# Optimization experiments

Hardware: AMD Instinct MI355X
Metric: run time of the kernel (lower is better)

## Reference

```python
import jax, jax.numpy as jnp
import numpy as np

HW, B, C, NH, NC, HF, WF = 2500, 2, 256, 8, 6, 64, 176
DFF = 4 * C
EPS = 1e-5

def _layernorm(x, g, b):
    m = x.mean(-1, keepdims=True)
    v = ((x - m) ** 2).mean(-1, keepdims=True)
    return (x - m) / jnp.sqrt(v + EPS) * g + b

def _mha(q, kv, in_w, in_b, ow, ob):
    # q: [L,B,C], kv: [S,B,C] (batch_first=False, torch nn.MultiheadAttention)
    L, Bq, Cq = q.shape
    S = kv.shape[0]
    Dh = Cq // NH
    qp = (q @ in_w[:Cq].T + in_b[:Cq]).reshape(L, Bq, NH, Dh)
    kp = (kv @ in_w[Cq:2 * Cq].T + in_b[Cq:2 * Cq]).reshape(S, Bq, NH, Dh)
    vp = (kv @ in_w[2 * Cq:].T + in_b[2 * Cq:]).reshape(S, Bq, NH, Dh)
    att = jnp.einsum('lbhd,sbhd->bhls', qp, kp) * (1.0 / np.sqrt(Dh))
    att = jax.nn.softmax(att, axis=-1)
    out = jnp.einsum('bhls,sbhd->lbhd', att, vp).reshape(L, Bq, Cq)
    return out @ ow.T + ob

def _grid_sample_zeros(feat, grid):
    # feat: [B,N,C,H,W], grid: [B,N,Q,2] in [-1,1]; bilinear, align_corners=False, zero padding
    Bb, N, Cc, Hf, Wf = feat.shape
    Q = grid.shape[2]
    x = (grid[..., 0] + 1.0) * (Wf / 2.0) - 0.5
    y = (grid[..., 1] + 1.0) * (Hf / 2.0) - 0.5
    x0 = jnp.floor(x); y0 = jnp.floor(y)
    wx = x - x0; wy = y - y0
    x0i = x0.astype(jnp.int32); y0i = y0.astype(jnp.int32)
    ff = feat.reshape(Bb, N, Cc, Hf * Wf)
    def corner(xi, yi, w):
        valid = (xi >= 0) & (xi < Wf) & (yi >= 0) & (yi < Hf)
        idx = jnp.clip(yi, 0, Hf - 1) * Wf + jnp.clip(xi, 0, Wf - 1)  # [B,N,Q]
        g = jnp.take_along_axis(ff, jnp.broadcast_to(idx[:, :, None, :], (Bb, N, Cc, Q)), axis=-1)
        return g * (w * valid)[:, :, None, :]
    return (corner(x0i, y0i, (1.0 - wx) * (1.0 - wy)) + corner(x0i + 1, y0i, wx * (1.0 - wy))
            + corner(x0i, y0i + 1, (1.0 - wx) * wy) + corner(x0i + 1, y0i + 1, wx * wy))

def _forward(bev_queries, prev_bev, image_feat, reference_points, camera_intrinsics, camera_extrinsics,
             in_proj_w, in_proj_b, out_proj_w, out_proj_b, tsa_norm_g, tsa_norm_b,
             sca_w, sca_b, sca_norm_g, sca_norm_b, ffn_w1, ffn_b1, ffn_w2, ffn_b2, ffn_norm_g, ffn_norm_b):
    # TSA (dropout is identity in eval)
    tsa_out = _mha(bev_queries, prev_bev, in_proj_w, in_proj_b, out_proj_w, out_proj_b)
    x = _layernorm(bev_queries + tsa_out, tsa_norm_g, tsa_norm_b)
    # SCA: ego->camera->image projection
    R = camera_extrinsics[:, :, :3, :3]            # [B,N,3,3]
    t = camera_extrinsics[:, :, :3, 3]             # [B,N,3]
    R_e2c = jnp.swapaxes(R, -1, -2)
    t_e2c = -jnp.einsum('bnij,bnj->bni', R_e2c, t)
    pts_cam = jnp.einsum('bnij,qj->bnqi', R_e2c, reference_points) + t_e2c[:, :, None, :]  # [B,N,Q,3]
    pts_img = jnp.einsum('bnij,bnqj->bnqi', camera_intrinsics, pts_cam)
    uv = pts_img[..., :2] / jnp.maximum(pts_img[..., 2:3], 1e-5)
    grid = jnp.stack([2.0 * uv[..., 0] / WF - 1.0, 2.0 * uv[..., 1] / HF - 1.0], axis=-1)  # [B,N,Q,2]
    Bq = bev_queries.shape[1]
    feat_r = image_feat.reshape(Bq, NC, C, HF, WF)
    sampled = _grid_sample_zeros(feat_r, grid).mean(axis=1)   # [B,C,Q]
    sampled = jnp.transpose(sampled, (2, 0, 1))               # [Q,B,C]
    sca_out = sampled @ sca_w.T + sca_b
    x = _layernorm(x + sca_out, sca_norm_g, sca_norm_b)
    # FFN (torch nn.GELU default = exact erf)
    h = jax.nn.gelu(x @ ffn_w1 + ffn_b1, approximate=False)
    ffn_out = h @ ffn_w2 + ffn_b2
    return _layernorm(x + ffn_out, ffn_norm_g, ffn_norm_b)

def setup_inputs():
    key = jax.random.key(0)
    ks = jax.random.split(key, 16)
    f = jnp.float32
    s = 0.02
    return {
        'bev_queries': jax.random.normal(ks[0], (HW, B, C), f),
        'prev_bev': jax.random.normal(ks[1], (HW, B, C), f),
        'image_feat': jax.random.normal(ks[2], (B * NC, C, HF, WF), f),
        'reference_points': jax.random.normal(ks[3], (HW, 3), f) * 20.0,
        'camera_intrinsics': jax.random.normal(ks[4], (B, NC, 3, 3), f),
        'camera_extrinsics': jax.random.normal(ks[5], (B, NC, 4, 4), f),
        'spatial_shapes': jnp.array([[HF, WF]], jnp.int32),
        'in_proj_w': jax.random.normal(ks[6], (3 * C, C), f) * s,
        'in_proj_b': jnp.zeros((3 * C,), f),
        'out_proj_w': jax.random.normal(ks[7], (C, C), f) * s,
        'out_proj_b': jnp.zeros((C,), f),
        'tsa_norm_g': jnp.ones((C,), f), 'tsa_norm_b': jnp.zeros((C,), f),
        'sca_w': jax.random.normal(ks[8], (C, C), f) * s,
        'sca_b': jnp.zeros((C,), f),
        'sca_norm_g': jnp.ones((C,), f), 'sca_norm_b': jnp.zeros((C,), f),
        'ffn_w1': jax.random.normal(ks[9], (C, DFF), f) * s,
        'ffn_b1': jnp.zeros((DFF,), f),
        'ffn_w2': jax.random.normal(ks[10], (DFF, C), f) * s,
        'ffn_b2': jnp.zeros((C,), f),
        'ffn_norm_g': jnp.ones((C,), f), 'ffn_norm_b': jnp.zeros((C,), f),
    }

def reference(bev_queries, prev_bev, image_feat, reference_points, camera_intrinsics, camera_extrinsics,
              in_proj_w, in_proj_b, out_proj_w, out_proj_b, tsa_norm_g, tsa_norm_b,
              sca_w, sca_b, sca_norm_g, sca_norm_b, ffn_w1, ffn_b1, ffn_w2, ffn_b2, ffn_norm_g, ffn_norm_b,
              spatial_shapes):
    return _forward(bev_queries, prev_bev, image_feat, reference_points, camera_intrinsics, camera_extrinsics,
                    in_proj_w, in_proj_b, out_proj_w, out_proj_b, tsa_norm_g, tsa_norm_b,
                    sca_w, sca_b, sca_norm_g, sca_norm_b, ffn_w1, ffn_b1, ffn_w2, ffn_b2, ffn_norm_g, ffn_norm_b)
```

## Files before the change

### kernel.cpp

```cpp
#include <hip/hip_runtime.h>

typedef unsigned short u16;
typedef __attribute__((ext_vector_type(8))) __bf16 bf8_t;
typedef __attribute__((ext_vector_type(4))) float f4_t;

__device__ __forceinline__ float bf2f(u16 v) {
  return __uint_as_float(((unsigned int)v) << 16);
}
__device__ __forceinline__ u16 f2bf(float f) {
  unsigned int u = __float_as_uint(f);
  unsigned int r = u + 0x7FFFu + ((u >> 16) & 1u);
  return (u16)(r >> 16);
}
__device__ __forceinline__ float bflo(unsigned int w) { return __uint_as_float(w << 16); }
__device__ __forceinline__ float bfhi(unsigned int w) { return __uint_as_float(w & 0xFFFF0000u); }

__device__ __forceinline__ void load8(const void* base, size_t off, int isf32, float v[8]) {
  if (isf32) {
    const float* p = (const float*)base + off;
    float4 a = *(const float4*)p, b = *(const float4*)(p + 4);
    v[0]=a.x; v[1]=a.y; v[2]=a.z; v[3]=a.w; v[4]=b.x; v[5]=b.y; v[6]=b.z; v[7]=b.w;
  } else {
    uint4 r = *(const uint4*)((const u16*)base + off);
    v[0]=bflo(r.x); v[1]=bfhi(r.x); v[2]=bflo(r.y); v[3]=bfhi(r.y);
    v[4]=bflo(r.z); v[5]=bfhi(r.z); v[6]=bflo(r.w); v[7]=bfhi(r.w);
  }
}
__device__ __forceinline__ float ldf1(const void* p, size_t i, int isf32) {
  return isf32 ? ((const float*)p)[i] : bf2f(((const u16*)p)[i]);
}

#define LQ   2500
#define BB   2
#define CC   256
#define DH   32
#define NCC  6
#define HFF  64
#define WFF  176
#define DFF  1024
#define MROWS 5000

#define WB_UV   256
#define WB_WQKV 240256
#define WB_WOP  633472
#define WB_WSC  764544
#define WB_WF1  895616
#define WB_WF2  1419904
#define WB_S1   1944192
#define WB_S2   (WB_S1 + 2621440)
#define WB_S3   (WB_S2 + 2621440)
#define WB_S4   (WB_S3 + 2621440)
#define WB_H    WB_S2
#define WB_Y3   (WB_S2 + 10485760)

__global__ void detect_k(const u16* __restrict__ rp, int* __restrict__ flag) {
  int bad = 0;
  for (int i = threadIdx.x; i < 7500; i += 64) {
    float v = bf2f(rp[i]);
    if (!(fabsf(v) < 1e6f)) bad = 1;
  }
  int anybad = __any(bad);
  if (threadIdx.x == 0) flag[0] = anybad ? 1 : 0;
}

struct WDesc {
  const void* src[5];
  u16* dst[5];
  int n[5];
  int mode[5];
  int Kd[5], Nd[5];
};
__global__ __launch_bounds__(256) void cvtw_k(WDesc d, const int* __restrict__ flag) {
  const int df = flag[0];
  const int i = blockIdx.y;
  const int n = d.n[i];
  for (int j = blockIdx.x * 256 + threadIdx.x; j < n; j += gridDim.x * 256) {
    float v;
    if (d.mode[i]) {
      const int K = d.Kd[i], N = d.Nd[i];
      const int nn = j / K, kk = j - nn * K;
      v = ldf1(d.src[i], (size_t)kk * N + nn, df);
    } else {
      v = ldf1(d.src[i], j, df);
    }
    d.dst[i][j] = f2bf(v);
  }
}

template<int XRAW, int ACT, int RES>
__global__ __launch_bounds__(256) void gemm_mf(
    const void* __restrict__ Xv, const u16* __restrict__ W,
    const void* __restrict__ bias, size_t boff,
    const void* __restrict__ resv,
    u16* __restrict__ Y, int M, int N, int K, const int* __restrict__ flag)
{
  const int df = flag[0];
  const int xf = XRAW ? df : 0;
  __shared__ __align__(16) u16 sA[64 * 32];
  __shared__ __align__(16) u16 sB[64 * 32];
  const int t = threadIdx.x;
  const int m0 = blockIdx.y * 64, n0 = blockIdx.x * 64;
  const int lane = t & 63, w = t >> 6;
  const int wr = w >> 1, wc = w & 1;
  const int ln15 = lane & 15, l4 = lane >> 4;

  f4_t acc[2][2];
#pragma unroll
  for (int a = 0; a < 2; ++a)
#pragma unroll
    for (int bq = 0; bq < 2; ++bq) acc[a][bq] = (f4_t){0.f, 0.f, 0.f, 0.f};

  const int srow = t >> 2, scol = (t & 3) * 8;
  for (int k0 = 0; k0 < K; k0 += 32) {
    {
      const int gm = m0 + srow;
      float v[8] = {0.f,0.f,0.f,0.f,0.f,0.f,0.f,0.f};
      if (gm < M) load8(Xv, (size_t)gm * K + k0 + scol, xf, v);
      uint4 o;
      o.x = (unsigned int)f2bf(v[0]) | ((unsigned int)f2bf(v[1]) << 16);
      o.y = (unsigned int)f2bf(v[2]) | ((unsigned int)f2bf(v[3]) << 16);
      o.z = (unsigned int)f2bf(v[4]) | ((unsigned int)f2bf(v[5]) << 16);
      o.w = (unsigned int)f2bf(v[6]) | ((unsigned int)f2bf(v[7]) << 16);
      *(uint4*)&sA[srow * 32 + scol] = o;
    }
    *(uint4*)&sB[srow * 32 + scol] =
        *(const uint4*)&W[(size_t)(n0 + srow) * K + k0 + scol];
    __syncthreads();
    bf8_t af[2], bf_[2];
    af[0]  = *(const bf8_t*)&sA[(wr * 32 + 0  + ln15) * 32 + l4 * 8];
    af[1]  = *(const bf8_t*)&sA[(wr * 32 + 16 + ln15) * 32 + l4 * 8];
    bf_[0] = *(const bf8_t*)&sB[(wc * 32 + 0  + ln15) * 32 + l4 * 8];
    bf_[1] = *(const bf8_t*)&sB[(wc * 32 + 16 + ln15) * 32 + l4 * 8];
#pragma unroll
    for (int mt = 0; mt < 2; ++mt)
#pragma unroll
      for (int nt = 0; nt < 2; ++nt)
        acc[mt][nt] = __builtin_amdgcn_mfma_f32_16x16x32_bf16(af[mt], bf_[nt], acc[mt][nt], 0, 0, 0);
    __syncthreads();
  }
#pragma unroll
  for (int nt = 0; nt < 2; ++nt) {
    const int gn = n0 + wc * 32 + nt * 16 + ln15;
    const float bv = ldf1(bias, boff + gn, df);
#pragma unroll
    for (int mt = 0; mt < 2; ++mt)
#pragma unroll
      for (int r = 0; r < 4; ++r) {
        const int gm = m0 + wr * 32 + mt * 16 + l4 * 4 + r;
        if (gm < M) {
          float x = acc[mt][nt][r] + bv;
          if (ACT) x = 0.5f * x * (1.f + erff(x * 0.70710678118654752f));
          if (RES == 1)      x += bf2f(((const u16*)resv)[(size_t)gm * N + gn]);
          else if (RES == 2) x += ldf1(resv, (size_t)gm * N + gn, df);
          Y[(size_t)gm * N + gn] = f2bf(x);
        }
      }
  }
}

__global__ __launch_bounds__(256) void attn_mf(
    const u16* __restrict__ Qw, const u16* __restrict__ Kw,
    const u16* __restrict__ Vw, u16* __restrict__ Ow)
{
  __shared__ __align__(16) u16 sQ[64 * 32];
  __shared__ __align__(16) u16 sK[64 * 32];
  __shared__ __align__(16) u16 sVT[32 * 72];
  __shared__ __align__(16) u16 sP[64 * 72];
  const int t = threadIdx.x;
  const int q0 = blockIdx.x * 64;
  const int b = blockIdx.y >> 3, h = blockIdx.y & 7;
  const int lane = t & 63, w = t >> 6;
  const int ln15 = lane & 15, l4 = lane >> 4;
  const float SC = 0.17677669529663687f;

  {
    const int qi = t >> 2, dcol = (t & 3) * 8;
    const size_t src = ((size_t)(q0 + qi) * BB + b) * CC + h * DH + dcol;
    *(uint4*)&sQ[qi * 32 + dcol] = *(const uint4*)&Qw[src];
  }

  f4_t oacc[2];
  oacc[0] = (f4_t){0.f,0.f,0.f,0.f};
  oacc[1] = (f4_t){0.f,0.f,0.f,0.f};
  float m_r[4] = {-1e30f, -1e30f, -1e30f, -1e30f};
  float l_r[4] = {0.f, 0.f, 0.f, 0.f};
  __syncthreads();

  for (int kt = 0; kt < 40; ++kt) {
    const int kbase = kt * 64;
    {
      const int j = t >> 2, dcol = (t & 3) * 8;
      const size_t src = ((size_t)(kbase + j) * BB + b) * CC + h * DH + dcol;
      *(uint4*)&sK[j * 32 + dcol] = *(const uint4*)&Kw[src];
      uint4 vv = *(const uint4*)&Vw[src];
      u16 ve[8];
      ve[0] = (u16)(vv.x & 0xffff); ve[1] = (u16)(vv.x >> 16);
      ve[2] = (u16)(vv.y & 0xffff); ve[3] = (u16)(vv.y >> 16);
      ve[4] = (u16)(vv.z & 0xffff); ve[5] = (u16)(vv.z >> 16);
      ve[6] = (u16)(vv.w & 0xffff); ve[7] = (u16)(vv.w >> 16);
#pragma unroll
      for (int x = 0; x < 8; ++x) sVT[(dcol + x) * 72 + j] = ve[x];
    }
    __syncthreads();

    bf8_t aq = *(const bf8_t*)&sQ[(w * 16 + ln15) * 32 + l4 * 8];
    f4_t sv[4];
#pragma unroll
    for (int nt = 0; nt < 4; ++nt) {
      bf8_t bk = *(const bf8_t*)&sK[(nt * 16 + ln15) * 32 + l4 * 8];
      f4_t z = (f4_t){0.f,0.f,0.f,0.f};
      sv[nt] = __builtin_amdgcn_mfma_f32_16x16x32_bf16(aq, bk, z, 0, 0, 0);
    }

    float p[4][4];
#pragma unroll
    for (int nt = 0; nt < 4; ++nt) {
      const bool ok = (kbase + nt * 16 + ln15) < LQ;
#pragma unroll
      for (int r = 0; r < 4; ++r)
        p[nt][r] = ok ? sv[nt][r] * SC : -1e30f;
    }
#pragma unroll
    for (int r = 0; r < 4; ++r) {
      float mloc = fmaxf(fmaxf(p[0][r], p[1][r]), fmaxf(p[2][r], p[3][r]));
      mloc = fmaxf(mloc, __shfl_xor(mloc, 1));
      mloc = fmaxf(mloc, __shfl_xor(mloc, 2));
      mloc = fmaxf(mloc, __shfl_xor(mloc, 4));
      mloc = fmaxf(mloc, __shfl_xor(mloc, 8));
      const float mn = fmaxf(m_r[r], mloc);
      const float alpha = __expf(m_r[r] - mn);
      m_r[r] = mn;
      float s = 0.f;
#pragma unroll
      for (int nt = 0; nt < 4; ++nt) { const float e = __expf(p[nt][r] - mn); p[nt][r] = e; s += e; }
      s += __shfl_xor(s, 1);
      s += __shfl_xor(s, 2);
      s += __shfl_xor(s, 4);
      s += __shfl_xor(s, 8);
      l_r[r] = l_r[r] * alpha + s;
      oacc[0][r] *= alpha;
      oacc[1][r] *= alpha;
    }

#pragma unroll
    for (int nt = 0; nt < 4; ++nt)
#pragma unroll
      for (int r = 0; r < 4; ++r)
        sP[(w * 16 + l4 * 4 + r) * 72 + nt * 16 + ln15] = f2bf(p[nt][r]);

#pragma unroll
    for (int ks = 0; ks < 2; ++ks) {
      bf8_t ap = *(const bf8_t*)&sP[(w * 16 + ln15) * 72 + ks * 32 + l4 * 8];
#pragma unroll
      for (int nt = 0; nt < 2; ++nt) {
        bf8_t bv = *(const bf8_t*)&sVT[(nt * 16 + ln15) * 72 + ks * 32 + l4 * 8];
        oacc[nt] = __builtin_amdgcn_mfma_f32_16x16x32_bf16(ap, bv, oacc[nt], 0, 0, 0);
      }
    }
    __syncthreads();
  }
#pragma unroll
  for (int nt = 0; nt < 2; ++nt)
#pragma unroll
    for (int r = 0; r < 4; ++r) {
      const int q = q0 + w * 16 + l4 * 4 + r;
      if (q < LQ) {
        const float val = oacc[nt][r] / l_r[r];
        Ow[((size_t)q * BB + b) * CC + h * DH + nt * 16 + ln15] = f2bf(val);
      }
    }
}

template<int TOOUT>
__global__ __launch_bounds__(256) void ln_k(const u16* __restrict__ X,
    const void* __restrict__ g, const void* __restrict__ be,
    void* __restrict__ Yv, int rows, const int* __restrict__ flag)
{
  const int df = flag[0];
  const int lane = threadIdx.x & 63;
  const int row = blockIdx.x * 4 + (threadIdx.x >> 6);
  if (row >= rows) return;
  uint2 raw = *(const uint2*)(X + (size_t)row * CC + lane * 4);
  float vx = bflo(raw.x), vy = bfhi(raw.x), vz = bflo(raw.y), vw = bfhi(raw.y);
  float s = vx + vy + vz + vw;
#pragma unroll
  for (int o = 1; o < 64; o <<= 1) s += __shfl_xor(s, o);
  const float mean = s * 0.00390625f;
  const float dx = vx - mean, dy = vy - mean, dz = vz - mean, dw = vw - mean;
  float sq = dx*dx + dy*dy + dz*dz + dw*dw;
#pragma unroll
  for (int o = 1; o < 64; o <<= 1) sq += __shfl_xor(sq, o);
  const float rstd = rsqrtf(sq * 0.00390625f + 1e-5f);
  const float g0 = ldf1(g, lane*4+0, df), g1 = ldf1(g, lane*4+1, df);
  const float g2 = ldf1(g, lane*4+2, df), g3 = ldf1(g, lane*4+3, df);
  const float b0 = ldf1(be, lane*4+0, df), b1 = ldf1(be, lane*4+1, df);
  const float b2 = ldf1(be, lane*4+2, df), b3 = ldf1(be, lane*4+3, df);
  const float y0 = dx * rstd * g0 + b0;
  const float y1 = dy * rstd * g1 + b1;
  const float y2 = dz * rstd * g2 + b2;
  const float y3 = dw * rstd * g3 + b3;
  if (TOOUT && df) {
    float* yp = (float*)Yv + (size_t)row * CC + lane * 4;
    *(float4*)yp = make_float4(y0, y1, y2, y3);
  } else {
    u16* yp = (u16*)Yv + (size_t)row * CC + lane * 4;
    unsigned int lo = (unsigned int)f2bf(y0) | ((unsigned int)f2bf(y1) << 16);
    unsigned int hi = (unsigned int)f2bf(y2) | ((unsigned int)f2bf(y3) << 16);
    *(uint2*)yp = make_uint2(lo, hi);
  }
}

__global__ __launch_bounds__(256) void uv_k(
    const void* __restrict__ refp, const void* __restrict__ intr,
    const void* __restrict__ extr, float* __restrict__ uv,
    const int* __restrict__ flag)
{
  const int df = flag[0];
  const int idx = blockIdx.x * 256 + threadIdx.x;
  if (idx >= BB * NCC * LQ) return;
  const int bc = idx / LQ;
  const int q = idx - bc * LQ;
  float R[3][3], tv[3], Kc[3][3], p[3];
#pragma unroll
  for (int i = 0; i < 3; ++i) {
#pragma unroll
    for (int j = 0; j < 3; ++j) {
      R[i][j] = ldf1(extr, bc*16 + i*4 + j, df);
      Kc[i][j] = ldf1(intr, bc*9 + i*3 + j, df);
    }
    tv[i] = ldf1(extr, bc*16 + i*4 + 3, df);
  }
#pragma unroll
  for (int j = 0; j < 3; ++j) p[j] = ldf1(refp, q*3 + j, df) - tv[j];
  float pc[3];
#pragma unroll
  for (int i = 0; i < 3; ++i) pc[i] = R[0][i]*p[0] + R[1][i]*p[1] + R[2][i]*p[2];
  float im[3];
#pragma unroll
  for (int i = 0; i < 3; ++i) im[i] = Kc[i][0]*pc[0] + Kc[i][1]*pc[1] + Kc[i][2]*pc[2];
  const float z = fmaxf(im[2], 1e-5f);
  uv[(size_t)idx*2 + 0] = im[0] / z - 0.5f;
  uv[(size_t)idx*2 + 1] = im[1] / z - 0.5f;
}

__global__ __launch_bounds__(256) void samp_k(
    const void* __restrict__ feat, const float* __restrict__ uv,
    u16* __restrict__ S, const int* __restrict__ flag)
{
  const int df = flag[0];
  const int c = blockIdx.x;
  const int b = blockIdx.y;
  for (int q = threadIdx.x; q < LQ; q += 256) {
    float acc = 0.f;
#pragma unroll
    for (int cam = 0; cam < NCC; ++cam) {
      const int bc = b * NCC + cam;
      const float x = uv[((size_t)bc * LQ + q) * 2 + 0];
      const float y = uv[((size_t)bc * LQ + q) * 2 + 1];
      const float xf = floorf(x), yf = floorf(y);
      const int x0 = (int)xf, y0 = (int)yf;
      const float wx = x - xf, wy = y - yf;
      const size_t base = ((size_t)bc * CC + c) * (HFF * WFF);
      const bool vx0 = (x0 >= 0) & (x0 < WFF);
      const bool vx1 = (x0 + 1 >= 0) & (x0 + 1 < WFF);
      const bool vy0 = (y0 >= 0) & (y0 < HFF);
      const bool vy1 = (y0 + 1 >= 0) & (y0 + 1 < HFF);
      if (vy0) {
        const size_t rb = base + (size_t)y0 * WFF;
        if (vx0) acc += (1.f - wx) * (1.f - wy) * ldf1(feat, rb + x0, df);
        if (vx1) acc += wx * (1.f - wy) * ldf1(feat, rb + x0 + 1, df);
      }
      if (vy1) {
        const size_t rb = base + (size_t)(y0 + 1) * WFF;
        if (vx0) acc += (1.f - wx) * wy * ldf1(feat, rb + x0, df);
        if (vx1) acc += wx * wy * ldf1(feat, rb + x0 + 1, df);
      }
    }
    S[((size_t)q * BB + b) * CC + c] = f2bf(acc * (1.f / 6.f));
  }
}

extern "C" void kernel_launch(void* const* d_in, const int* in_sizes, int n_in,
                              void* d_out, int out_size, void* d_ws, size_t ws_size,
                              hipStream_t stream) {
  (void)in_sizes; (void)n_in; (void)out_size; (void)ws_size;
  char* base = (char*)d_ws;
  int* flag = (int*)base;
  float* UV = (float*)(base + WB_UV);
  u16* WQKV = (u16*)(base + WB_WQKV);
  u16* WOP  = (u16*)(base + WB_WOP);
  u16* WSC  = (u16*)(base + WB_WSC);
  u16* WF1  = (u16*)(base + WB_WF1);
  u16* WF2  = (u16*)(base + WB_WF2);
  u16* S1 = (u16*)(base + WB_S1);
  u16* S2 = (u16*)(base + WB_S2);
  u16* S3 = (u16*)(base + WB_S3);
  u16* S4 = (u16*)(base + WB_S4);
  u16* H  = (u16*)(base + WB_H);
  u16* Y3 = (u16*)(base + WB_Y3);

  detect_k<<<1, 64, 0, stream>>>((const u16*)d_in[3], flag);

  WDesc wd;
  wd.src[0] = d_in[7];  wd.dst[0] = WQKV; wd.n[0] = 196608; wd.mode[0] = 0; wd.Kd[0] = 0;    wd.Nd[0] = 0;
  wd.src[1] = d_in[9];  wd.dst[1] = WOP;  wd.n[1] = 65536;  wd.mode[1] = 0; wd.Kd[1] = 0;    wd.Nd[1] = 0;
  wd.src[2] = d_in[13]; wd.dst[2] = WSC;  wd.n[2] = 65536;  wd.mode[2] = 0; wd.Kd[2] = 0;    wd.Nd[2] = 0;
  wd.src[3] = d_in[17]; wd.dst[3] = WF1;  wd.n[3] = 262144; wd.mode[3] = 1; wd.Kd[3] = 256;  wd.Nd[3] = 1024;
  wd.src[4] = d_in[19]; wd.dst[4] = WF2;  wd.n[4] = 262144; wd.mode[4] = 1; wd.Kd[4] = 1024; wd.Nd[4] = 256;
  cvtw_k<<<dim3(256, 5), 256, 0, stream>>>(wd, flag);

  uv_k<<<(BB * NCC * LQ + 255) / 256, 256, 0, stream>>>(d_in[3], d_in[4], d_in[5], UV, flag);

  gemm_mf<1,0,0><<<dim3(4, 79), 256, 0, stream>>>(d_in[0], WQKV,          d_in[8], 0,   nullptr, S1, MROWS, CC, CC, flag);
  gemm_mf<1,0,0><<<dim3(4, 79), 256, 0, stream>>>(d_in[1], WQKV + 65536,  d_in[8], 256, nullptr, S2, MROWS, CC, CC, flag);
  gemm_mf<1,0,0><<<dim3(4, 79), 256, 0, stream>>>(d_in[1], WQKV + 131072, d_in[8], 512, nullptr, S3, MROWS, CC, CC, flag);

  attn_mf<<<dim3(40, 16), 256, 0, stream>>>(S1, S2, S3, S4);

  gemm_mf<0,0,2><<<dim3(4, 79), 256, 0, stream>>>(S4, WOP, d_in[10], 0, d_in[0], S1, MROWS, CC, CC, flag);
  ln_k<0><<<1250, 256, 0, stream>>>(S1, d_in[11], d_in[12], S2, MROWS, flag);

  samp_k<<<dim3(CC, BB), 256, 0, stream>>>(d_in[2], UV, S3, flag);

  gemm_mf<0,0,1><<<dim3(4, 79), 256, 0, stream>>>(S3, WSC, d_in[14], 0, S2, S4, MROWS, CC, CC, flag);
  ln_k<0><<<1250, 256, 0, stream>>>(S4, d_in[15], d_in[16], S1, MROWS, flag);

  gemm_mf<0,1,0><<<dim3(16, 79), 256, 0, stream>>>(S1, WF1, d_in[18], 0, nullptr, H,  MROWS, DFF, CC,  flag);
  gemm_mf<0,0,1><<<dim3(4, 79),  256, 0, stream>>>(H,  WF2, d_in[20], 0, S1,      Y3, MROWS, CC, DFF, flag);
  ln_k<1><<<1250, 256, 0, stream>>>(Y3, d_in[21], d_in[22], d_out, MROWS, flag);
}
```

Measured before the change: 545.5 us.

## Rework GEMMs to LDS-free single-wave tiles and stream K/V directly in attention

Every GEMM becomes a single-wavefront kernel that reads A and B fragments straight from global memory into MFMA operands, with no LDS staging or barriers. The V projection now writes a transposed, padded layout so attention can load K and V^T fragments directly from global memory. Attention folds the softmax scale and log2(e) into Q so it can use exp2. The sampling kernel's grid is split five ways along queries to add parallelism. This removes barriers and LDS traffic, but data reuse across waves now relies on cache hits, and the transposed V store is scattered.

```diff
diff --git a/kernel.cpp b/kernel.cpp
--- a/kernel.cpp
+++ b/kernel.cpp
@@ -3,6 +3,8 @@
 typedef unsigned short u16;
 typedef __attribute__((ext_vector_type(8))) __bf16 bf8_t;
 typedef __attribute__((ext_vector_type(4))) float f4_t;
+
+union bf8u { u16 u[8]; bf8_t v; uint4 q; };
 
 __device__ __forceinline__ float bf2f(u16 v) {
   return __uint_as_float(((unsigned int)v) << 16);
@@ -14,30 +16,18 @@
 }
 __device__ __forceinline__ float bflo(unsigned int w) { return __uint_as_float(w << 16); }
 __device__ __forceinline__ float bfhi(unsigned int w) { return __uint_as_float(w & 0xFFFF0000u); }
-
-__device__ __forceinline__ void load8(const void* base, size_t off, int isf32, float v[8]) {
-  if (isf32) {
-    const float* p = (const float*)base + off;
-    float4 a = *(const float4*)p, b = *(const float4*)(p + 4);
-    v[0]=a.x; v[1]=a.y; v[2]=a.z; v[3]=a.w; v[4]=b.x; v[5]=b.y; v[6]=b.z; v[7]=b.w;
-  } else {
-    uint4 r = *(const uint4*)((const u16*)base + off);
-    v[0]=bflo(r.x); v[1]=bfhi(r.x); v[2]=bflo(r.y); v[3]=bfhi(r.y);
-    v[4]=bflo(r.z); v[5]=bfhi(r.z); v[6]=bflo(r.w); v[7]=bfhi(r.w);
-  }
-}
 __device__ __forceinline__ float ldf1(const void* p, size_t i, int isf32) {
   return isf32 ? ((const float*)p)[i] : bf2f(((const u16*)p)[i]);
 }
 
-#define LQ   2500
-#define BB   2
-#define CC   256
-#define DH   32
-#define NCC  6
-#define HFF  64
-#define WFF  176
-#define DFF  1024
+#define LQ    2500
+#define LQP   2560
+#define BB    2
+#define CC    256
+#define NCC   6
+#define HFF   64
+#define WFF   176
+#define DFF   1024
 #define MROWS 5000
 
 #define WB_UV   256
@@ -49,7 +39,7 @@
 #define WB_S1   1944192
 #define WB_S2   (WB_S1 + 2621440)
 #define WB_S3   (WB_S2 + 2621440)
-#define WB_S4   (WB_S3 + 2621440)
+#define WB_VT   (WB_S3 + 2621440)
 #define WB_H    WB_S2
 #define WB_Y3   (WB_S2 + 10485760)
 
@@ -64,119 +54,103 @@
 }
 
 struct WDesc {
-  const void* src[5];
-  u16* dst[5];
-  int n[5];
-  int mode[5];
-  int Kd[5], Nd[5];
+  const void* src[6];
+  u16* dst[6];
+  int n[6];
+  int mode[6];
+  int Kd[6], Nd[6];
 };
 __global__ __launch_bounds__(256) void cvtw_k(WDesc d, const int* __restrict__ flag) {
   const int df = flag[0];
   const int i = blockIdx.y;
   const int n = d.n[i];
   for (int j = blockIdx.x * 256 + threadIdx.x; j < n; j += gridDim.x * 256) {
-    float v;
-    if (d.mode[i]) {
+    if (d.mode[i] == 2) {
+      const int row = j / (LQP - LQ), col = LQ + j % (LQP - LQ);
+      d.dst[i][(size_t)row * LQP + col] = 0;
+    } else if (d.mode[i] == 1) {
       const int K = d.Kd[i], N = d.Nd[i];
       const int nn = j / K, kk = j - nn * K;
-      v = ldf1(d.src[i], (size_t)kk * N + nn, df);
+      d.dst[i][j] = f2bf(ldf1(d.src[i], (size_t)kk * N + nn, df));
     } else {
-      v = ldf1(d.src[i], j, df);
-    }
-    d.dst[i][j] = f2bf(v);
-  }
-}
-
-template<int XRAW, int ACT, int RES>
-__global__ __launch_bounds__(256) void gemm_mf(
+      d.dst[i][j] = f2bf(ldf1(d.src[i], j, df));
+    }
+  }
+}
+
+template<int XRAW, int ACT, int RES, int STORE_T>
+__global__ __launch_bounds__(64) void gemm_nl(
     const void* __restrict__ Xv, const u16* __restrict__ W,
     const void* __restrict__ bias, size_t boff,
     const void* __restrict__ resv,
     u16* __restrict__ Y, int M, int N, int K, const int* __restrict__ flag)
 {
   const int df = flag[0];
-  const int xf = XRAW ? df : 0;
-  __shared__ __align__(16) u16 sA[64 * 32];
-  __shared__ __align__(16) u16 sB[64 * 32];
-  const int t = threadIdx.x;
-  const int m0 = blockIdx.y * 64, n0 = blockIdx.x * 64;
-  const int lane = t & 63, w = t >> 6;
-  const int wr = w >> 1, wc = w & 1;
+  const int lane = threadIdx.x;
   const int ln15 = lane & 15, l4 = lane >> 4;
-
-  f4_t acc[2][2];
-#pragma unroll
-  for (int a = 0; a < 2; ++a)
-#pragma unroll
-    for (int bq = 0; bq < 2; ++bq) acc[a][bq] = (f4_t){0.f, 0.f, 0.f, 0.f};
-
-  const int srow = t >> 2, scol = (t & 3) * 8;
+  const int m0 = blockIdx.x * 16, n0 = blockIdx.y * 64;
+  const int am = min(m0 + ln15, M - 1);
+
+  f4_t acc[4];
+#pragma unroll
+  for (int nt = 0; nt < 4; ++nt) acc[nt] = (f4_t){0.f, 0.f, 0.f, 0.f};
+
   for (int k0 = 0; k0 < K; k0 += 32) {
-    {
-      const int gm = m0 + srow;
-      float v[8] = {0.f,0.f,0.f,0.f,0.f,0.f,0.f,0.f};
-      if (gm < M) load8(Xv, (size_t)gm * K + k0 + scol, xf, v);
-      uint4 o;
-      o.x = (unsigned int)f2bf(v[0]) | ((unsigned int)f2bf(v[1]) << 16);
-      o.y = (unsigned int)f2bf(v[2]) | ((unsigned int)f2bf(v[3]) << 16);
-      o.z = (unsigned int)f2bf(v[4]) | ((unsigned int)f2bf(v[5]) << 16);
-      o.w = (unsigned int)f2bf(v[6]) | ((unsigned int)f2bf(v[7]) << 16);
-      *(uint4*)&sA[srow * 32 + scol] = o;
-    }
-    *(uint4*)&sB[srow * 32 + scol] =
-        *(const uint4*)&W[(size_t)(n0 + srow) * K + k0 + scol];
-    __syncthreads();
-    bf8_t af[2], bf_[2];
-    af[0]  = *(const bf8_t*)&sA[(wr * 32 + 0  + ln15) * 32 + l4 * 8];
-    af[1]  = *(const bf8_t*)&sA[(wr * 32 + 16 + ln15) * 32 + l4 * 8];
-    bf_[0] = *(const bf8_t*)&sB[(wc * 32 + 0  + ln15) * 32 + l4 * 8];
-    bf_[1] = *(const bf8_t*)&sB[(wc * 32 + 16 + ln15) * 32 + l4 * 8];
-#pragma unroll
-    for (int mt = 0; mt < 2; ++mt)
-#pragma unroll
-      for (int nt = 0; nt < 2; ++nt)
-        acc[mt][nt] = __builtin_amdgcn_mfma_f32_16x16x32_bf16(af[mt], bf_[nt], acc[mt][nt], 0, 0, 0);
-    __syncthreads();
-  }
-#pragma unroll
-  for (int nt = 0; nt < 2; ++nt) {
-    const int gn = n0 + wc * 32 + nt * 16 + ln15;
+    bf8u a;
+    if (XRAW && df) {
+      const float* p = (const float*)Xv + (size_t)am * K + k0 + l4 * 8;
+      float4 r0 = *(const float4*)p, r1 = *(const float4*)(p + 4);
+      a.u[0]=f2bf(r0.x); a.u[1]=f2bf(r0.y); a.u[2]=f2bf(r0.z); a.u[3]=f2bf(r0.w);
+      a.u[4]=f2bf(r1.x); a.u[5]=f2bf(r1.y); a.u[6]=f2bf(r1.z); a.u[7]=f2bf(r1.w);
+    } else {
+      a.q = *(const uint4*)((const u16*)Xv + (size_t)am * K + k0 + l4 * 8);
+    }
+#pragma unroll
+    for (int nt = 0; nt < 4; ++nt) {
+      bf8u b;
+      b.q = *(const uint4*)&W[(size_t)(n0 + nt * 16 + ln15) * K + k0 + l4 * 8];
+      acc[nt] = __builtin_amdgcn_mfma_f32_16x16x32_bf16(a.v, b.v, acc[nt], 0, 0, 0);
+    }
+  }
+#pragma unroll
+  for (int nt = 0; nt < 4; ++nt) {
+    const int gn = n0 + nt * 16 + ln15;
     const float bv = ldf1(bias, boff + gn, df);
 #pragma unroll
-    for (int mt = 0; mt < 2; ++mt)
-#pragma unroll
-      for (int r = 0; r < 4; ++r) {
-        const int gm = m0 + wr * 32 + mt * 16 + l4 * 4 + r;
-        if (gm < M) {
-          float x = acc[mt][nt][r] + bv;
-          if (ACT) x = 0.5f * x * (1.f + erff(x * 0.70710678118654752f));
-          if (RES == 1)      x += bf2f(((const u16*)resv)[(size_t)gm * N + gn]);
-          else if (RES == 2) x += ldf1(resv, (size_t)gm * N + gn, df);
-          Y[(size_t)gm * N + gn] = f2bf(x);
-        }
-      }
+    for (int r = 0; r < 4; ++r) {
+      const int gm = m0 + l4 * 4 + r;
+      if (gm < M) {
+        float x = acc[nt][r] + bv;
+        if (ACT) x = 0.5f * x * (1.f + erff(x * 0.70710678118654752f));
+        if (RES == 1)      x += bf2f(((const u16*)resv)[(size_t)gm * N + gn]);
+        else if (RES == 2) x += ldf1(resv, (size_t)gm * N + gn, df);
+        if (STORE_T) Y[(size_t)(gn + (gm & 1) * 256) * LQP + (gm >> 1)] = f2bf(x);
+        else         Y[(size_t)gm * N + gn] = f2bf(x);
+      }
+    }
   }
 }
 
 __global__ __launch_bounds__(256) void attn_mf(
     const u16* __restrict__ Qw, const u16* __restrict__ Kw,
-    const u16* __restrict__ Vw, u16* __restrict__ Ow)
-{
-  __shared__ __align__(16) u16 sQ[64 * 32];
-  __shared__ __align__(16) u16 sK[64 * 32];
-  __shared__ __align__(16) u16 sVT[32 * 72];
-  __shared__ __align__(16) u16 sP[64 * 72];
+    const u16* __restrict__ Vt, u16* __restrict__ Ow)
+{
+  __shared__ __align__(16) u16 sP[4][16 * 72];
   const int t = threadIdx.x;
-  const int q0 = blockIdx.x * 64;
-  const int b = blockIdx.y >> 3, h = blockIdx.y & 7;
   const int lane = t & 63, w = t >> 6;
   const int ln15 = lane & 15, l4 = lane >> 4;
-  const float SC = 0.17677669529663687f;
-
+  const int q0 = blockIdx.x * 64 + w * 16;
+  const int by = blockIdx.y;
+  const int b = by >> 3, h = by & 7;
+  u16* myP = &sP[w][0];
+  const float SCL2E = 0.25505654481f;
+
+  bf8u aq;
   {
-    const int qi = t >> 2, dcol = (t & 3) * 8;
-    const size_t src = ((size_t)(q0 + qi) * BB + b) * CC + h * DH + dcol;
-    *(uint4*)&sQ[qi * 32 + dcol] = *(const uint4*)&Qw[src];
+    const size_t qaddr = ((size_t)(q0 + ln15) * BB + b) * CC + h * 32 + l4 * 8;
+    bf8u qr; qr.q = *(const uint4*)&Qw[qaddr];
+#pragma unroll
+    for (int i = 0; i < 8; ++i) aq.u[i] = f2bf(bf2f(qr.u[i]) * SCL2E);
   }
 
   f4_t oacc[2];
@@ -184,41 +158,23 @@
   oacc[1] = (f4_t){0.f,0.f,0.f,0.f};
   float m_r[4] = {-1e30f, -1e30f, -1e30f, -1e30f};
   float l_r[4] = {0.f, 0.f, 0.f, 0.f};
-  __syncthreads();
 
   for (int kt = 0; kt < 40; ++kt) {
-    const int kbase = kt * 64;
-    {
-      const int j = t >> 2, dcol = (t & 3) * 8;
-      const size_t src = ((size_t)(kbase + j) * BB + b) * CC + h * DH + dcol;
-      *(uint4*)&sK[j * 32 + dcol] = *(const uint4*)&Kw[src];
-      uint4 vv = *(const uint4*)&Vw[src];
-      u16 ve[8];
-      ve[0] = (u16)(vv.x & 0xffff); ve[1] = (u16)(vv.x >> 16);
-      ve[2] = (u16)(vv.y & 0xffff); ve[3] = (u16)(vv.y >> 16);
-      ve[4] = (u16)(vv.z & 0xffff); ve[5] = (u16)(vv.z >> 16);
-      ve[6] = (u16)(vv.w & 0xffff); ve[7] = (u16)(vv.w >> 16);
-#pragma unroll
-      for (int x = 0; x < 8; ++x) sVT[(dcol + x) * 72 + j] = ve[x];
-    }
-    __syncthreads();
-
-    bf8_t aq = *(const bf8_t*)&sQ[(w * 16 + ln15) * 32 + l4 * 8];
+    const int kb = kt * 64;
     f4_t sv[4];
 #pragma unroll
     for (int nt = 0; nt < 4; ++nt) {
-      bf8_t bk = *(const bf8_t*)&sK[(nt * 16 + ln15) * 32 + l4 * 8];
+      bf8u bk;
+      bk.q = *(const uint4*)&Kw[((size_t)(kb + nt * 16 + ln15) * BB + b) * CC + h * 32 + l4 * 8];
       f4_t z = (f4_t){0.f,0.f,0.f,0.f};
-      sv[nt] = __builtin_amdgcn_mfma_f32_16x16x32_bf16(aq, bk, z, 0, 0, 0);
-    }
-
+      sv[nt] = __builtin_amdgcn_mfma_f32_16x16x32_bf16(aq.v, bk.v, z, 0, 0, 0);
+    }
     float p[4][4];
 #pragma unroll
     for (int nt = 0; nt < 4; ++nt) {
-      const bool ok = (kbase + nt * 16 + ln15) < LQ;
-#pragma unroll
-      for (int r = 0; r < 4; ++r)
-        p[nt][r] = ok ? sv[nt][r] * SC : -1e30f;
+      const bool ok = (kb + nt * 16 + ln15) < LQ;
+#pragma unroll
+      for (int r = 0; r < 4; ++r) p[nt][r] = ok ? sv[nt][r] : -1e30f;
     }
 #pragma unroll
     for (int r = 0; r < 4; ++r) {
@@ -228,11 +184,14 @@
       mloc = fmaxf(mloc, __shfl_xor(mloc, 4));
       mloc = fmaxf(mloc, __shfl_xor(mloc, 8));
       const float mn = fmaxf(m_r[r], mloc);
-      const float alpha = __expf(m_r[r] - mn);
+      const float alpha = __builtin_amdgcn_exp2f(m_r[r] - mn);
       m_r[r] = mn;
       float s = 0.f;
 #pragma unroll
-      for (int nt = 0; nt < 4; ++nt) { const float e = __expf(p[nt][r] - mn); p[nt][r] = e; s += e; }
+      for (int nt = 0; nt < 4; ++nt) {
+        const float e = __builtin_amdgcn_exp2f(p[nt][r] - mn);
+        p[nt][r] = e; s += e;
+      }
       s += __shfl_xor(s, 1);
       s += __shfl_xor(s, 2);
       s += __shfl_xor(s, 4);
@@ -241,32 +200,31 @@
       oacc[0][r] *= alpha;
       oacc[1][r] *= alpha;
     }
-
 #pragma unroll
     for (int nt = 0; nt < 4; ++nt)
 #pragma unroll
       for (int r = 0; r < 4; ++r)
-        sP[(w * 16 + l4 * 4 + r) * 72 + nt * 16 + ln15] = f2bf(p[nt][r]);
-
+        myP[(l4 * 4 + r) * 72 + nt * 16 + ln15] = f2bf(p[nt][r]);
 #pragma unroll
     for (int ks = 0; ks < 2; ++ks) {
-      bf8_t ap = *(const bf8_t*)&sP[(w * 16 + ln15) * 72 + ks * 32 + l4 * 8];
+      bf8u ap;
+      ap.q = *(const uint4*)&myP[ln15 * 72 + ks * 32 + l4 * 8];
 #pragma unroll
       for (int nt = 0; nt < 2; ++nt) {
-        bf8_t bv = *(const bf8_t*)&sVT[(nt * 16 + ln15) * 72 + ks * 32 + l4 * 8];
-        oacc[nt] = __builtin_amdgcn_mfma_f32_16x16x32_bf16(ap, bv, oacc[nt], 0, 0, 0);
-      }
-    }
-    __syncthreads();
+        bf8u bv;
+        bv.q = *(const uint4*)&Vt[(size_t)(by * 32 + nt * 16 + ln15) * LQP + kb + ks * 32 + l4 * 8];
+        oacc[nt] = __builtin_amdgcn_mfma_f32_16x16x32_bf16(ap.v, bv.v, oacc[nt], 0, 0, 0);
+      }
+    }
   }
 #pragma unroll
   for (int nt = 0; nt < 2; ++nt)
 #pragma unroll
     for (int r = 0; r < 4; ++r) {
-      const int q = q0 + w * 16 + l4 * 4 + r;
+      const int q = q0 + l4 * 4 + r;
       if (q < LQ) {
         const float val = oacc[nt][r] / l_r[r];
-        Ow[((size_t)q * BB + b) * CC + h * DH + nt * 16 + ln15] = f2bf(val);
+        Ow[((size_t)q * BB + b) * CC + h * 32 + nt * 16 + ln15] = f2bf(val);
       }
     }
 }
@@ -349,8 +307,10 @@
 {
   const int df = flag[0];
   const int c = blockIdx.x;
-  const int b = blockIdx.y;
-  for (int q = threadIdx.x; q < LQ; q += 256) {
+  const int b = blockIdx.y / 5;
+  const int ch = blockIdx.y % 5;
+  const int qend = min((ch + 1) * 500, LQ);
+  for (int q = ch * 500 + threadIdx.x; q < qend; q += 256) {
     float acc = 0.f;
 #pragma unroll
     for (int cam = 0; cam < NCC; ++cam) {
@@ -395,7 +355,7 @@
   u16* S1 = (u16*)(base + WB_S1);
   u16* S2 = (u16*)(base + WB_S2);
   u16* S3 = (u16*)(base + WB_S3);
-  u16* S4 = (u16*)(base + WB_S4);
+  u16* VT = (u16*)(base + WB_VT);
   u16* H  = (u16*)(base + WB_H);
   u16* Y3 = (u16*)(base + WB_Y3);
 
@@ -407,25 +367,26 @@
   wd.src[2] = d_in[13]; wd.dst[2] = WSC;  wd.n[2] = 65536;  wd.mode[2] = 0; wd.Kd[2] = 0;    wd.Nd[2] = 0;
   wd.src[3] = d_in[17]; wd.dst[3] = WF1;  wd.n[3] = 262144; wd.mode[3] = 1; wd.Kd[3] = 256;  wd.Nd[3] = 1024;
   wd.src[4] = d_in[19]; wd.dst[4] = WF2;  wd.n[4] = 262144; wd.mode[4] = 1; wd.Kd[4] = 1024; wd.Nd[4] = 256;
-  cvtw_k<<<dim3(256, 5), 256, 0, stream>>>(wd, flag);
+  wd.src[5] = nullptr;  wd.dst[5] = VT;   wd.n[5] = 512 * (LQP - LQ); wd.mode[5] = 2; wd.Kd[5] = 0; wd.Nd[5] = 0;
+  cvtw_k<<<dim3(128, 6), 256, 0, stream>>>(wd, flag);
 
   uv_k<<<(BB * NCC * LQ + 255) / 256, 256, 0, stream>>>(d_in[3], d_in[4], d_in[5], UV, flag);
 
-  gemm_mf<1,0,0><<<dim3(4, 79), 256, 0, stream>>>(d_in[0], WQKV,          d_in[8], 0,   nullptr, S1, MROWS, CC, CC, flag);
-  gemm_mf<1,0,0><<<dim3(4, 79), 256, 0, stream>>>(d_in[1], WQKV + 65536,  d_in[8], 256, nullptr, S2, MROWS, CC, CC, flag);
-  gemm_mf<1,0,0><<<dim3(4, 79), 256, 0, stream>>>(d_in[1], WQKV + 131072, d_in[8], 512, nullptr, S3, MROWS, CC, CC, flag);
-
-  attn_mf<<<dim3(40, 16), 256, 0, stream>>>(S1, S2, S3, S4);
-
-  gemm_mf<0,0,2><<<dim3(4, 79), 256, 0, stream>>>(S4, WOP, d_in[10], 0, d_in[0], S1, MROWS, CC, CC, flag);
+  gemm_nl<1,0,0,0><<<dim3(313, 4), 64, 0, stream>>>(d_in[0], WQKV,          d_in[8], 0,   nullptr, S1, MROWS, CC, CC, flag);
+  gemm_nl<1,0,0,0><<<dim3(313, 4), 64, 0, stream>>>(d_in[1], WQKV + 65536,  d_in[8], 256, nullptr, S2, MROWS, CC, CC, flag);
+  gemm_nl<1,0,0,1><<<dim3(313, 4), 64, 0, stream>>>(d_in[1], WQKV + 131072, d_in[8], 512, nullptr, VT, MROWS, CC, CC, flag);
+
+  attn_mf<<<dim3(40, 16), 256, 0, stream>>>(S1, S2, VT, S3);
+
+  gemm_nl<0,0,2,0><<<dim3(313, 4), 64, 0, stream>>>(S3, WOP, d_in[10], 0, d_in[0], S1, MROWS, CC, CC, flag);
   ln_k<0><<<1250, 256, 0, stream>>>(S1, d_in[11], d_in[12], S2, MROWS, flag);
 
-  samp_k<<<dim3(CC, BB), 256, 0, stream>>>(d_in[2], UV, S3, flag);
-
-  gemm_mf<0,0,1><<<dim3(4, 79), 256, 0, stream>>>(S3, WSC, d_in[14], 0, S2, S4, MROWS, CC, CC, flag);
-  ln_k<0><<<1250, 256, 0, stream>>>(S4, d_in[15], d_in[16], S1, MROWS, flag);
-
-  gemm_mf<0,1,0><<<dim3(16, 79), 256, 0, stream>>>(S1, WF1, d_in[18], 0, nullptr, H,  MROWS, DFF, CC,  flag);
-  gemm_mf<0,0,1><<<dim3(4, 79),  256, 0, stream>>>(H,  WF2, d_in[20], 0, S1,      Y3, MROWS, CC, DFF, flag);
+  samp_k<<<dim3(CC, BB * 5), 256, 0, stream>>>(d_in[2], UV, VT, flag);
+
+  gemm_nl<0,0,1,0><<<dim3(313, 4), 64, 0, stream>>>(VT, WSC, d_in[14], 0, S2, S3, MROWS, CC, CC, flag);
+  ln_k<0><<<1250, 256, 0, stream>>>(S3, d_in[15], d_in[16], S1, MROWS, flag);
+
+  gemm_nl<0,1,0,0><<<dim3(313, 16), 64, 0, stream>>>(S1, WF1, d_in[18], 0, nullptr, H,  MROWS, DFF, CC,  flag);
+  gemm_nl<0,0,1,0><<<dim3(313, 4),  64, 0, stream>>>(H,  WF2, d_in[20], 0, S1,      Y3, MROWS, CC,  DFF, flag);
   ln_k<1><<<1250, 256, 0, stream>>>(Y3, d_in[21], d_in[22], d_out, MROWS, flag);
 }
```

Result: slower. 564.1 us (+3.4%).
